# Kernel optimization log

Measured on AMD Instinct MI355X. Metric: run time of the kernel, lower is better.

Reference implementation:

```python
import jax, jax.numpy as jnp
import numpy as np

D = 1024
H = 16
HD = D // H
EPS = 1e-5


def layer_norm(x, g, b):
    mu = jnp.mean(x, axis=-1, keepdims=True)
    var = jnp.var(x, axis=-1, keepdims=True)
    return (x - mu) * jax.lax.rsqrt(var + EPS) * g + b


def setup_inputs() -> dict:
    key = jax.random.key(0)
    ks = jax.random.split(key, 16)
    s = 0.02
    return {
        "x": jax.random.normal(ks[0], (2, 2048, D), jnp.float32),
        "ln1_g": jnp.ones((D,), jnp.float32),
        "ln1_b": jnp.zeros((D,), jnp.float32),
        "Wq": jax.random.normal(ks[1], (D, D), jnp.float32) * s,
        "bq": jnp.zeros((D,), jnp.float32),
        "Wk": jax.random.normal(ks[2], (D, D), jnp.float32) * s,
        "bk": jnp.zeros((D,), jnp.float32),
        "Wv": jax.random.normal(ks[3], (D, D), jnp.float32) * s,
        "bv": jnp.zeros((D,), jnp.float32),
        "Wo": jax.random.normal(ks[4], (D, D), jnp.float32) * s,
        "bo": jnp.zeros((D,), jnp.float32),
        "ln2_g": jnp.ones((D,), jnp.float32),
        "ln2_b": jnp.zeros((D,), jnp.float32),
        "W1": jax.random.normal(ks[5], (D, 4 * D), jnp.float32) * s,
        "b1": jnp.zeros((4 * D,), jnp.float32),
        "W2": jax.random.normal(ks[6], (4 * D, D), jnp.float32) * s,
        "b2": jnp.zeros((D,), jnp.float32),
    }


def reference(x, ln1_g, ln1_b, Wq, bq, Wk, bk, Wv, bv, Wo, bo, ln2_g, ln2_b, W1, b1, W2, b2):
    B, T, _ = x.shape
    # --- attention sub-block (pre-LN) ---
    h = layer_norm(x, ln1_g, ln1_b)
    q = (h @ Wq + bq).reshape(B, T, H, HD).transpose(0, 2, 1, 3)  # [B,H,T,hd]
    k = (h @ Wk + bk).reshape(B, T, H, HD).transpose(0, 2, 1, 3)
    v = (h @ Wv + bv).reshape(B, T, H, HD).transpose(0, 2, 1, 3)
    scores = jnp.einsum("bhqd,bhkd->bhqk", q, k)  # full O(T^2) scores as in source
    causal = jnp.tril(jnp.ones((T, T), bool))
    scores = jnp.where(causal, scores, -jnp.inf)
    w = jax.nn.softmax(scores / np.sqrt(HD), axis=-1)
    ctx = jnp.einsum("bhqk,bhkd->bhqd", w, v)
    ctx = ctx.transpose(0, 2, 1, 3).reshape(B, T, D)
    x = x + (ctx @ Wo + bo)
    # --- MLP sub-block (pre-LN) ---
    h = layer_norm(x, ln2_g, ln2_b)
    h = jax.nn.gelu(h @ W1 + b1, approximate=False)
    x = x + (h @ W2 + b2)
    return x
```

## Files before the change

kernel.cpp:

```cpp
#include <hip/hip_runtime.h>
#include <math.h>


typedef _Float16 half8 __attribute__((ext_vector_type(8)));
typedef _Float16 half4v __attribute__((ext_vector_type(4)));
typedef float floatx4 __attribute__((ext_vector_type(4)));

#define DMODEL 1024
#define SEQT   2048
#define NTOK   4096
#define NHEAD  16
#define HDIM   64

__device__ __forceinline__ void llds16(const _Float16* g, _Float16* l) {
  __builtin_amdgcn_global_load_lds(
      (const __attribute__((address_space(1))) void*)g,
      (__attribute__((address_space(3))) void*)l, 16, 0, 0);
}

__global__ __launch_bounds__(256) void wtrans_kernel(
    const float* __restrict__ Wq, const float* __restrict__ Wk,
    const float* __restrict__ Wv, const float* __restrict__ Wo,
    const float* __restrict__ W1, const float* __restrict__ W2,
    _Float16* __restrict__ wt_base) {
  __shared__ float tilebuf[32][33];
  int id = blockIdx.x;
  const float* src; _Float16* dst; int K, N, t;
  if (id < 4096) {
    int s = id >> 10;
    src = (s == 0) ? Wq : (s == 1) ? Wk : (s == 2) ? Wv : Wo;
    dst = wt_base + (size_t)s * (1024 * 1024);
    K = 1024; N = 1024; t = id & 1023;
  } else if (id < 8192) {
    src = W1; dst = wt_base + (size_t)4 * 1024 * 1024; K = 1024; N = 4096; t = id - 4096;
  } else {
    src = W2; dst = wt_base + (size_t)8 * 1024 * 1024; K = 4096; N = 1024; t = id - 8192;
  }
  int tilesN = N >> 5;
  int tk = t / tilesN, tn = t % tilesN;
  int c = threadIdx.x & 31, r0 = threadIdx.x >> 5;
#pragma unroll
  for (int i = 0; i < 4; ++i) {
    int r = r0 + i * 8;
    tilebuf[r][c] = src[(size_t)(tk * 32 + r) * N + tn * 32 + c];
  }
  __syncthreads();
#pragma unroll
  for (int i = 0; i < 4; ++i) {
    int r = r0 + i * 8;
    dst[(size_t)(tn * 32 + r) * K + tk * 32 + c] = (_Float16)tilebuf[c][r];
  }
}

__global__ __launch_bounds__(256) void ln_kernel(
    const float* __restrict__ x, const float* __restrict__ g,
    const float* __restrict__ b, _Float16* __restrict__ out) {
  int row = blockIdx.x;
  int t = threadIdx.x;
  const float4 xv = ((const float4*)(x + (size_t)row * DMODEL))[t];
  float s = xv.x + xv.y + xv.z + xv.w;
  float s2 = xv.x * xv.x + xv.y * xv.y + xv.z * xv.z + xv.w * xv.w;
#pragma unroll
  for (int off = 32; off; off >>= 1) {
    s += __shfl_down(s, off);
    s2 += __shfl_down(s2, off);
  }
  __shared__ float red[8];
  int wid = t >> 6;
  if ((t & 63) == 0) { red[wid] = s; red[wid + 4] = s2; }
  __syncthreads();
  s = red[0] + red[1] + red[2] + red[3];
  s2 = red[4] + red[5] + red[6] + red[7];
  float mu = s * (1.0f / DMODEL);
  float var = s2 * (1.0f / DMODEL) - mu * mu;
  float rstd = rsqrtf(var + 1e-5f);
  const float4 gv = ((const float4*)g)[t];
  const float4 bv = ((const float4*)b)[t];
  half4v o;
  o[0] = (_Float16)((xv.x - mu) * rstd * gv.x + bv.x);
  o[1] = (_Float16)((xv.y - mu) * rstd * gv.y + bv.y);
  o[2] = (_Float16)((xv.z - mu) * rstd * gv.z + bv.z);
  o[3] = (_Float16)((xv.w - mu) * rstd * gv.w + bv.w);
  *(half4v*)(out + (size_t)row * DMODEL + t * 4) = o;
}

template <int MODE>
__global__ __launch_bounds__(256) void gemm_kernel(
    const _Float16* __restrict__ A, const _Float16* __restrict__ Bt0, int K,
    const float* __restrict__ bias0, const float* __restrict__ bias1,
    const float* __restrict__ bias2, const float* __restrict__ res,
    float* __restrict__ outf, _Float16* __restrict__ outh) {
  constexpr int NT = (MODE == 1) ? 64 : 128;
  constexpr int MI = (NT == 128) ? 4 : 2;
  constexpr int BCH = NT / 64;
  __shared__ __align__(16) _Float16 As[2][128 * 32];
  __shared__ __align__(16) _Float16 Bs[2][NT * 32];
  const int tid = threadIdx.x;
  const int m0 = blockIdx.x * 128;
  const _Float16* Bt;
  const float* bias;
  _Float16* outh_sel = outh;
  int n0, sel = 0;
  if (MODE == 0) {
    sel = blockIdx.y >> 3;
    n0 = (blockIdx.y & 7) * 128;
    Bt = Bt0 + (size_t)sel * (1024 * 1024);
    bias = (sel == 0) ? bias0 : (sel == 1) ? bias1 : bias2;
    outh_sel = outh + (size_t)sel * ((size_t)NTOK * DMODEL);
  } else {
    n0 = blockIdx.y * NT;
    Bt = Bt0;
    bias = bias0;
  }
  const int w = tid >> 6, lane = tid & 63;
  const int l15 = lane & 15, q8 = lane >> 4;
  const int wrow = (NT == 128) ? (w >> 1) * 64 : w * 32;
  const int wcol = (NT == 128) ? (w & 1) * 64 : 0;
  const int csw = (q8 ^ ((l15 >> 1) & 3)) * 8;

  const _Float16* gA[2]; int ldsA[2];
  const _Float16* gB[BCH]; int ldsB[BCH];
#pragma unroll
  for (int i = 0; i < 2; ++i) {
    int c0 = i * 256 + w * 64;
    int idx = c0 + lane;
    int m = idx >> 2;
    int kq = ((idx & 3) ^ ((m >> 1) & 3)) * 8;
    gA[i] = A + (size_t)(m0 + m) * K + kq;
    ldsA[i] = c0 * 8;
  }
#pragma unroll
  for (int i = 0; i < BCH; ++i) {
    int c0 = i * 256 + w * 64;
    int idx = c0 + lane;
    int m = idx >> 2;
    int kq = ((idx & 3) ^ ((m >> 1) & 3)) * 8;
    gB[i] = Bt + (size_t)(n0 + m) * K + kq;
    ldsB[i] = c0 * 8;
  }

  auto stage = [&](int buf) {
#pragma unroll
    for (int i = 0; i < 2; ++i) {
      llds16(gA[i], &As[buf][ldsA[i]]);
      gA[i] += 32;
    }
#pragma unroll
    for (int i = 0; i < BCH; ++i) {
      llds16(gB[i], &Bs[buf][ldsB[i]]);
      gB[i] += 32;
    }
  };

  floatx4 acc[MI][4];
#pragma unroll
  for (int i = 0; i < MI; ++i)
#pragma unroll
    for (int j = 0; j < 4; ++j) acc[i][j] = (floatx4){0.f, 0.f, 0.f, 0.f};

  const int nk = K >> 5;
  stage(0);
  __syncthreads();
  for (int t = 0; t < nk; ++t) {
    const int buf = t & 1;
    if (t + 1 < nk) stage(buf ^ 1);
    half8 af[MI], bf[4];
#pragma unroll
    for (int i = 0; i < MI; ++i)
      af[i] = *(const half8*)&As[buf][(wrow + i * 16 + l15) * 32 + csw];
#pragma unroll
    for (int j = 0; j < 4; ++j)
      bf[j] = *(const half8*)&Bs[buf][(wcol + j * 16 + l15) * 32 + csw];
#pragma unroll
    for (int i = 0; i < MI; ++i)
#pragma unroll
      for (int j = 0; j < 4; ++j)
        acc[i][j] = __builtin_amdgcn_mfma_f32_16x16x32_f16(af[i], bf[j], acc[i][j], 0, 0, 0);
    __syncthreads();
  }

#pragma unroll
  for (int i = 0; i < MI; ++i) {
    int rowb = m0 + wrow + i * 16 + q8 * 4;
#pragma unroll
    for (int j = 0; j < 4; ++j) {
      int col = n0 + wcol + j * 16 + l15;
      float bval = bias[col];
#pragma unroll
      for (int r = 0; r < 4; ++r) {
        int row = rowb + r;
        float v = acc[i][j][r] + bval;
        if (MODE == 0) {
          int bb = row >> 11, tt = row & 2047;
          int hh = col >> 6, hd = col & 63;
          if (sel == 2)
            outh_sel[((size_t)(bb * NHEAD + hh) * HDIM + hd) * SEQT + tt] = (_Float16)v;
          else
            outh_sel[((size_t)(bb * NHEAD + hh) * SEQT + tt) * HDIM + hd] = (_Float16)v;
        } else if (MODE == 1) {
          v += res[(size_t)row * 1024 + col];
          outf[(size_t)row * 1024 + col] = v;
        } else {
          float z = 1.5957691216f * v * (1.0f + 0.044715f * v * v);
          float gl = v / (1.0f + __expf(-z));
          outh[(size_t)row * 4096 + col] = (_Float16)gl;
        }
      }
    }
  }
}

__global__ __launch_bounds__(256) void attn_kernel(
    const _Float16* __restrict__ q, const _Float16* __restrict__ k,
    const _Float16* __restrict__ vt, _Float16* __restrict__ ctx) {
  __shared__ __align__(16) _Float16 Ks[2][64 * 64];
  __shared__ __align__(16) _Float16 Vs[2][64 * 64];
  __shared__ __align__(16) _Float16 Ps[64 * 72];
  __shared__ float Lpart[4][64];
  const int tid = threadIdx.x;
  const int w = tid >> 6, lane = tid & 63;
  const int l15 = lane & 15, q8 = lane >> 4;
  const int bh = blockIdx.y;
  const int pr = blockIdx.x;
  const size_t base = (size_t)bh * SEQT * HDIM;

  const _Float16* gk0[2]; const _Float16* gv0[2]; int ldsc[2];
#pragma unroll
  for (int i = 0; i < 2; ++i) {
    int c = i * 256 + w * 64 + lane;
    int r = c >> 3, gc = ((c & 7) ^ (r & 7)) * 8;
    gk0[i] = k + base + (size_t)r * HDIM + gc;
    gv0[i] = vt + base + (size_t)r * SEQT + gc;
    ldsc[i] = c * 8;
  }
  auto stage = [&](int kt, int buf) {
#pragma unroll
    for (int i = 0; i < 2; ++i) {
      llds16(gk0[i] + (size_t)kt * (64 * HDIM), &Ks[buf][ldsc[i]]);
      llds16(gv0[i] + kt * 64, &Vs[buf][ldsc[i]]);
    }
  };

  const int rswA = (l15 & 7);
  const int cs0 = (q8 ^ rswA) * 8;
  const int cs1 = ((4 + q8) ^ rswA) * 8;

  int s = 0;
  stage(0, 0);
  __syncthreads();
  for (int ph = 0; ph < 2; ++ph) {
    const int qtile = ph ? 31 - pr : pr;
    const int ntile = qtile + 1;
    half8 bq[4][2];
#pragma unroll
    for (int nt = 0; nt < 4; ++nt) {
      const half8* qp = (const half8*)(q + base + (size_t)(qtile * 64 + nt * 16 + l15) * HDIM);
      bq[nt][0] = qp[q8];
      bq[nt][1] = qp[4 + q8];
    }
    floatx4 acc[4];
#pragma unroll
    for (int j = 0; j < 4; ++j) acc[j] = (floatx4){0.f, 0.f, 0.f, 0.f};
    float lsum[4] = {0.f, 0.f, 0.f, 0.f};

    for (int jt = 0; jt < ntile; ++jt, ++s) {
      const int buf = s & 1;
      if (s + 1 < 33) {
        int sn = s + 1;
        int nkt = (sn <= pr) ? sn : sn - (pr + 1);
        stage(nkt, buf ^ 1);
      }
      half8 ak0 = *(const half8*)&Ks[buf][(w * 16 + l15) * 64 + cs0];
      half8 ak1 = *(const half8*)&Ks[buf][(w * 16 + l15) * 64 + cs1];
      floatx4 sv[4];
#pragma unroll
      for (int nt = 0; nt < 4; ++nt) {
        sv[nt] = __builtin_amdgcn_mfma_f32_16x16x32_f16(ak0, bq[nt][0],
                                                        (floatx4){0.f, 0.f, 0.f, 0.f}, 0, 0, 0);
        sv[nt] = __builtin_amdgcn_mfma_f32_16x16x32_f16(ak1, bq[nt][1], sv[nt], 0, 0, 0);
      }
      const bool diag = (jt == ntile - 1);
#pragma unroll
      for (int nt = 0; nt < 4; ++nt) {
        half4v phv;
#pragma unroll
        for (int r = 0; r < 4; ++r) {
          float p = __expf(sv[nt][r] * 0.125f);
          if (diag) {
            p = (w * 16 + q8 * 4 + r <= nt * 16 + l15) ? p : 0.f;
          }
          lsum[nt] += p;
          phv[r] = (_Float16)p;
        }
        *(half4v*)&Ps[(nt * 16 + l15) * 72 + w * 16 + q8 * 4] = phv;
      }
      __syncthreads();
      half8 ap0 = *(const half8*)&Ps[(w * 16 + l15) * 72 + q8 * 8];
      half8 ap1 = *(const half8*)&Ps[(w * 16 + l15) * 72 + 32 + q8 * 8];
#pragma unroll
      for (int ntd = 0; ntd < 4; ++ntd) {
        half8 bv0 = *(const half8*)&Vs[buf][(ntd * 16 + l15) * 64 + cs0];
        half8 bv1 = *(const half8*)&Vs[buf][(ntd * 16 + l15) * 64 + cs1];
        acc[ntd] = __builtin_amdgcn_mfma_f32_16x16x32_f16(ap0, bv0, acc[ntd], 0, 0, 0);
        acc[ntd] = __builtin_amdgcn_mfma_f32_16x16x32_f16(ap1, bv1, acc[ntd], 0, 0, 0);
      }
      __syncthreads();
    }

#pragma unroll
    for (int nt = 0; nt < 4; ++nt) {
      lsum[nt] += __shfl_xor(lsum[nt], 16);
      lsum[nt] += __shfl_xor(lsum[nt], 32);
      if (q8 == 0) Lpart[w][nt * 16 + l15] = lsum[nt];
    }
    __syncthreads();
    const int b = bh >> 4, h = bh & 15;
#pragma unroll
    for (int r = 0; r < 4; ++r) {
      int qr = w * 16 + q8 * 4 + r;
      float inv = 1.0f / (Lpart[0][qr] + Lpart[1][qr] + Lpart[2][qr] + Lpart[3][qr]);
      int tg = qtile * 64 + qr;
      _Float16* op = ctx + ((size_t)(b * SEQT + tg)) * DMODEL + h * HDIM;
#pragma unroll
      for (int ntd = 0; ntd < 4; ++ntd)
        op[ntd * 16 + l15] = (_Float16)(acc[ntd][r] * inv);
    }
  }
}

extern "C" void kernel_launch(void* const* d_in, const int* in_sizes, int n_in,
                              void* d_out, int out_size, void* d_ws, size_t ws_size,
                              hipStream_t stream) {
  (void)in_sizes; (void)n_in; (void)out_size; (void)ws_size;
  const float* x    = (const float*)d_in[0];
  const float* ln1g = (const float*)d_in[1];
  const float* ln1b = (const float*)d_in[2];
  const float* Wq   = (const float*)d_in[3];
  const float* bq   = (const float*)d_in[4];
  const float* Wk   = (const float*)d_in[5];
  const float* bk   = (const float*)d_in[6];
  const float* Wv   = (const float*)d_in[7];
  const float* bv   = (const float*)d_in[8];
  const float* Wo   = (const float*)d_in[9];
  const float* bo   = (const float*)d_in[10];
  const float* ln2g = (const float*)d_in[11];
  const float* ln2b = (const float*)d_in[12];
  const float* W1   = (const float*)d_in[13];
  const float* b1   = (const float*)d_in[14];
  const float* W2   = (const float*)d_in[15];
  const float* b2   = (const float*)d_in[16];
  float* out = (float*)d_out;

  char* ws = (char*)d_ws;
  _Float16* wt    = (_Float16*)(ws);
  _Float16* h16   = (_Float16*)(ws + ((size_t)24 << 20));
  _Float16* qkv   = (_Float16*)(ws + ((size_t)32 << 20));
  _Float16* ctx16 = (_Float16*)(ws + ((size_t)24 << 20));
  float*    x1    = (float*)   (ws + ((size_t)32 << 20));
  _Float16* h2    = (_Float16*)(ws + ((size_t)48 << 20));
  _Float16* mid   = (_Float16*)(ws + ((size_t)56 << 20));

  const size_t QKV1 = (size_t)NTOK * DMODEL;

  wtrans_kernel<<<12288, 256, 0, stream>>>(Wq, Wk, Wv, Wo, W1, W2, wt);
  ln_kernel<<<NTOK, 256, 0, stream>>>(x, ln1g, ln1b, h16);
  gemm_kernel<0><<<dim3(32, 24), 256, 0, stream>>>(
      h16, wt, 1024, bq, bk, bv, nullptr, nullptr, qkv);
  attn_kernel<<<dim3(16, 32), 256, 0, stream>>>(
      qkv, qkv + QKV1, qkv + 2 * QKV1, ctx16);
  gemm_kernel<1><<<dim3(32, 16), 256, 0, stream>>>(
      ctx16, wt + (size_t)3 * 1024 * 1024, 1024, bo, nullptr, nullptr, x, x1, nullptr);
  ln_kernel<<<NTOK, 256, 0, stream>>>(x1, ln2g, ln2b, h2);
  gemm_kernel<2><<<dim3(32, 32), 256, 0, stream>>>(
      h2, wt + (size_t)4 * 1024 * 1024, 1024, b1, nullptr, nullptr, nullptr, nullptr, mid);
  gemm_kernel<1><<<dim3(32, 16), 256, 0, stream>>>(
      mid, wt + (size_t)8 * 1024 * 1024, 4096, b2, nullptr, nullptr, x1, out, nullptr);
}
```

Baseline: 355.4 us.

## Use 4-deep LDS pipeline with single barrier for MODE 1 GEMM

For the MODE 1 GEMM (NT=64), the LDS staging grows from double to quadruple buffering with a prefetch distance of two. Explicit vmcnt waits plus one s_barrier per iteration replace the trailing __syncthreads, letting global-to-LDS loads overlap more compute. In the attention kernel, a __syncthreads is replaced by an lgkmcnt wait and a raw barrier, which leaves outstanding global loads unwaited. This costs more LDS per block and depends on the hand-counted vmcnt values matching the number of loads each stage issues.

```diff
diff --git a/kernel.cpp b/kernel.cpp
--- a/kernel.cpp
+++ b/kernel.cpp
@@ -93,8 +93,9 @@
   constexpr int NT = (MODE == 1) ? 64 : 128;
   constexpr int MI = (NT == 128) ? 4 : 2;
   constexpr int BCH = NT / 64;
-  __shared__ __align__(16) _Float16 As[2][128 * 32];
-  __shared__ __align__(16) _Float16 Bs[2][NT * 32];
+  constexpr int NBUF = (MODE == 1) ? 4 : 2;
+  __shared__ __align__(16) _Float16 As[NBUF][128 * 32];
+  __shared__ __align__(16) _Float16 Bs[NBUF][NT * 32];
   const int tid = threadIdx.x;
   const int m0 = blockIdx.x * 128;
   const _Float16* Bt;
@@ -159,24 +160,55 @@
     for (int j = 0; j < 4; ++j) acc[i][j] = (floatx4){0.f, 0.f, 0.f, 0.f};
 
   const int nk = K >> 5;
-  stage(0);
-  __syncthreads();
-  for (int t = 0; t < nk; ++t) {
-    const int buf = t & 1;
-    if (t + 1 < nk) stage(buf ^ 1);
-    half8 af[MI], bf[4];
-#pragma unroll
-    for (int i = 0; i < MI; ++i)
-      af[i] = *(const half8*)&As[buf][(wrow + i * 16 + l15) * 32 + csw];
-#pragma unroll
-    for (int j = 0; j < 4; ++j)
-      bf[j] = *(const half8*)&Bs[buf][(wcol + j * 16 + l15) * 32 + csw];
-#pragma unroll
-    for (int i = 0; i < MI; ++i)
+  if constexpr (MODE == 1) {
+    stage(0);
+    stage(1);
+    for (int t = 0; t < nk; ++t) {
+      const int buf = t & 3;
+      if (t + 2 < nk) {
+        stage((t + 2) & 3);
+        asm volatile("s_waitcnt vmcnt(6)" ::: "memory");
+      } else if (t + 1 < nk) {
+        asm volatile("s_waitcnt vmcnt(3)" ::: "memory");
+      } else {
+        asm volatile("s_waitcnt vmcnt(0)" ::: "memory");
+      }
+      __builtin_amdgcn_s_barrier();
+      asm volatile("" ::: "memory");
+      half8 af[MI], bf[4];
+#pragma unroll
+      for (int i = 0; i < MI; ++i)
+        af[i] = *(const half8*)&As[buf][(wrow + i * 16 + l15) * 32 + csw];
 #pragma unroll
       for (int j = 0; j < 4; ++j)
-        acc[i][j] = __builtin_amdgcn_mfma_f32_16x16x32_f16(af[i], bf[j], acc[i][j], 0, 0, 0);
+        bf[j] = *(const half8*)&Bs[buf][(wcol + j * 16 + l15) * 32 + csw];
+#pragma unroll
+      for (int i = 0; i < MI; ++i)
+#pragma unroll
+        for (int j = 0; j < 4; ++j)
+          acc[i][j] = __builtin_amdgcn_mfma_f32_16x16x32_f16(af[i], bf[j], acc[i][j], 0, 0, 0);
+      asm volatile("" ::: "memory");
+    }
+  } else {
+    stage(0);
     __syncthreads();
+    for (int t = 0; t < nk; ++t) {
+      const int buf = t & 1;
+      if (t + 1 < nk) stage(buf ^ 1);
+      half8 af[MI], bf[4];
+#pragma unroll
+      for (int i = 0; i < MI; ++i)
+        af[i] = *(const half8*)&As[buf][(wrow + i * 16 + l15) * 32 + csw];
+#pragma unroll
+      for (int j = 0; j < 4; ++j)
+        bf[j] = *(const half8*)&Bs[buf][(wcol + j * 16 + l15) * 32 + csw];
+#pragma unroll
+      for (int i = 0; i < MI; ++i)
+#pragma unroll
+        for (int j = 0; j < 4; ++j)
+          acc[i][j] = __builtin_amdgcn_mfma_f32_16x16x32_f16(af[i], bf[j], acc[i][j], 0, 0, 0);
+      __syncthreads();
+    }
   }
 
 #pragma unroll
@@ -294,7 +326,9 @@
         }
         *(half4v*)&Ps[(nt * 16 + l15) * 72 + w * 16 + q8 * 4] = phv;
       }
-      __syncthreads();
+      asm volatile("s_waitcnt lgkmcnt(0)" ::: "memory");
+      __builtin_amdgcn_s_barrier();
+      asm volatile("" ::: "memory");
       half8 ap0 = *(const half8*)&Ps[(w * 16 + l15) * 72 + q8 * 8];
       half8 ap1 = *(const half8*)&Ps[(w * 16 + l15) * 72 + 32 + q8 * 8];
 #pragma unroll
```

After: 354.2 us. About the same (-0.3%).

## Add 256x256-tile pipelined GEMM for MLP with split-K down-projection

Applied to the files above, without the earlier changes.

Adds a new 512-thread GEMM kernel with 256x256 tiles, K-step 64, XOR-swizzled LDS staged by direct global-to-LDS loads, and phased MFMA quadrants under barriers and s_setprio. It replaces both MLP GEMMs. The W2 GEMM is split four ways along K, with three partial sums stored in fp16 and added by a new reduction kernel. The attention kernel's post-P-store __syncthreads is swapped for an explicit lgkmcnt wait plus s_barrier. The aim is more data reuse per tile and better MFMA/load overlap, at the cost of an extra launch, extra partial-sum traffic and fp16 rounding of the partials.

```diff
diff --git a/kernel.cpp b/kernel.cpp
--- a/kernel.cpp
+++ b/kernel.cpp
@@ -82,6 +82,184 @@
   o[2] = (_Float16)((xv.z - mu) * rstd * gv.z + bv.z);
   o[3] = (_Float16)((xv.w - mu) * rstd * gv.w + bv.w);
   *(half4v*)(out + (size_t)row * DMODEL + t * 4) = o;
+}
+
+template <int OUTMODE>
+__global__ __launch_bounds__(512, 2) void gemm256_kernel(
+    const _Float16* __restrict__ A, const _Float16* __restrict__ Bt, int K,
+    const float* __restrict__ bias, const float* __restrict__ res,
+    float* __restrict__ outf, _Float16* __restrict__ outh,
+    _Float16* __restrict__ p1, _Float16* __restrict__ p2,
+    _Float16* __restrict__ p3) {
+  __shared__ __align__(16) _Float16 As[2][256 * 64];
+  __shared__ __align__(16) _Float16 Bs[2][256 * 64];
+  const int tid = threadIdx.x;
+  const int w = tid >> 6, lane = tid & 63;
+  const int l15 = lane & 15, q8 = lane >> 4;
+  const int wr = w >> 2, wc = w & 3;
+  const int m0 = blockIdx.x * 256;
+  const int n0 = blockIdx.y * 256;
+  int Keff = K, koff = 0;
+  if (OUTMODE == 1) { Keff = K >> 2; koff = blockIdx.z * Keff; }
+  const int nk = Keff >> 6;
+
+  auto stage_half = [&](int kt, int buf, int h) {
+#pragma unroll
+    for (int o = 0; o < 2; ++o) {
+      int cl = o * 512 + tid;
+      int rr = cl >> 3;
+      int m = h * 128 + rr;
+      int sc = (cl & 7) ^ (m & 7);
+      llds16(A + (size_t)(m0 + m) * K + koff + kt * 64 + sc * 8,
+             &As[buf][h * 8192 + cl * 8]);
+    }
+#pragma unroll
+    for (int o = 0; o < 2; ++o) {
+      int cl = o * 512 + tid;
+      int rr = cl >> 3;
+      int m = h * 128 + rr;
+      int sc = (cl & 7) ^ (m & 7);
+      llds16(Bt + (size_t)(n0 + m) * K + koff + kt * 64 + sc * 8,
+             &Bs[buf][h * 8192 + cl * 8]);
+    }
+  };
+
+  floatx4 acc[8][4];
+#pragma unroll
+  for (int i = 0; i < 8; ++i)
+#pragma unroll
+    for (int j = 0; j < 4; ++j) acc[i][j] = (floatx4){0.f, 0.f, 0.f, 0.f};
+
+  half8 a[4][2], b[2][2];
+
+#define DSA(BUF, R2)                                                         \
+  {                                                                          \
+    _Pragma("unroll") for (int i = 0; i < 4; ++i) {                          \
+      int rA = wr * 128 + (R2)*64 + i * 16 + l15;                            \
+      _Pragma("unroll") for (int kh = 0; kh < 2; ++kh) {                     \
+        int slot = (kh * 4 + q8) ^ (rA & 7);                                 \
+        a[i][kh] = *(const half8*)&As[BUF][rA * 64 + slot * 8];              \
+      }                                                                      \
+    }                                                                        \
+  }
+#define DSB(BUF, C2)                                                         \
+  {                                                                          \
+    _Pragma("unroll") for (int j = 0; j < 2; ++j) {                          \
+      int rB = wc * 64 + (C2)*32 + j * 16 + l15;                             \
+      _Pragma("unroll") for (int kh = 0; kh < 2; ++kh) {                     \
+        int slot = (kh * 4 + q8) ^ (rB & 7);                                 \
+        b[j][kh] = *(const half8*)&Bs[BUF][rB * 64 + slot * 8];              \
+      }                                                                      \
+    }                                                                        \
+  }
+#define MFMAQ(R2, C2)                                                        \
+  {                                                                          \
+    _Pragma("unroll") for (int i = 0; i < 4; ++i)                            \
+        _Pragma("unroll") for (int j = 0; j < 2; ++j)                        \
+            _Pragma("unroll") for (int kh = 0; kh < 2; ++kh)                 \
+                acc[(R2)*4 + i][(C2)*2 + j] =                                \
+        __builtin_amdgcn_mfma_f32_16x16x32_f16(a[i][kh], b[j][kh],           \
+                                               acc[(R2)*4 + i][(C2)*2 + j], \
+                                               0, 0, 0);                     \
+  }
+#define PH_SYNC()                                           \
+  __builtin_amdgcn_s_barrier();                             \
+  asm volatile("s_waitcnt lgkmcnt(0)" ::: "memory");        \
+  __builtin_amdgcn_sched_barrier(0);                        \
+  __builtin_amdgcn_s_setprio(1);
+#define PH_END()                                            \
+  __builtin_amdgcn_s_setprio(0);                            \
+  __builtin_amdgcn_s_barrier();
+
+  stage_half(0, 0, 0);
+  stage_half(0, 0, 1);
+  if (nk > 1) {
+    stage_half(1, 1, 0);
+    asm volatile("s_waitcnt vmcnt(4)" ::: "memory");
+  } else {
+    asm volatile("s_waitcnt vmcnt(0)" ::: "memory");
+  }
+  __builtin_amdgcn_s_barrier();
+
+  for (int kt = 0; kt < nk; ++kt) {
+    const int buf = kt & 1;
+    DSA(buf, 0);
+    DSB(buf, 0);
+    if (kt + 1 < nk) stage_half(kt + 1, buf ^ 1, 1);
+    PH_SYNC();
+    MFMAQ(0, 0);
+    PH_END();
+    DSB(buf, 1);
+    PH_SYNC();
+    MFMAQ(0, 1);
+    PH_END();
+    DSA(buf, 1);
+    DSB(buf, 0);
+    PH_SYNC();
+    MFMAQ(1, 0);
+    PH_END();
+    DSB(buf, 1);
+    PH_SYNC();
+    MFMAQ(1, 1);
+    __builtin_amdgcn_s_setprio(0);
+    __builtin_amdgcn_s_barrier();
+    if (kt + 2 < nk) stage_half(kt + 2, buf, 0);
+    if (kt + 1 < nk) {
+      asm volatile("s_waitcnt vmcnt(4)" ::: "memory");
+    } else {
+      asm volatile("s_waitcnt vmcnt(0)" ::: "memory");
+    }
+    __builtin_amdgcn_s_barrier();
+  }
+#undef DSA
+#undef DSB
+#undef MFMAQ
+#undef PH_SYNC
+#undef PH_END
+
+#pragma unroll
+  for (int fi = 0; fi < 8; ++fi) {
+    int rowb = m0 + wr * 128 + fi * 16 + q8 * 4;
+#pragma unroll
+    for (int fj = 0; fj < 4; ++fj) {
+      int col = n0 + wc * 64 + fj * 16 + l15;
+      float bval = bias[col];
+#pragma unroll
+      for (int r = 0; r < 4; ++r) {
+        int row = rowb + r;
+        float v = acc[fi][fj][r];
+        if (OUTMODE == 0) {
+          v += bval;
+          float z = 1.5957691216f * v * (1.0f + 0.044715f * v * v);
+          float gl = v / (1.0f + __expf(-z));
+          outh[(size_t)row * 4096 + col] = (_Float16)gl;
+        } else {
+          if (blockIdx.z == 0) {
+            v += bval + res[(size_t)row * 1024 + col];
+            outf[(size_t)row * 1024 + col] = v;
+          } else {
+            _Float16* pp = (blockIdx.z == 1) ? p1 : (blockIdx.z == 2) ? p2 : p3;
+            pp[(size_t)row * 1024 + col] = (_Float16)v;
+          }
+        }
+      }
+    }
+  }
+}
+
+__global__ __launch_bounds__(256) void redux_kernel(
+    float* __restrict__ out, const _Float16* __restrict__ p1,
+    const _Float16* __restrict__ p2, const _Float16* __restrict__ p3) {
+  size_t i = ((size_t)blockIdx.x * 256 + threadIdx.x) * 4;
+  float4 o = *(float4*)(out + i);
+  half4v a = *(const half4v*)(p1 + i);
+  half4v b = *(const half4v*)(p2 + i);
+  half4v c = *(const half4v*)(p3 + i);
+  o.x += (float)a[0] + (float)b[0] + (float)c[0];
+  o.y += (float)a[1] + (float)b[1] + (float)c[1];
+  o.z += (float)a[2] + (float)b[2] + (float)c[2];
+  o.w += (float)a[3] + (float)b[3] + (float)c[3];
+  *(float4*)(out + i) = o;
 }
 
 template <int MODE>
@@ -197,13 +375,9 @@
             outh_sel[((size_t)(bb * NHEAD + hh) * HDIM + hd) * SEQT + tt] = (_Float16)v;
           else
             outh_sel[((size_t)(bb * NHEAD + hh) * SEQT + tt) * HDIM + hd] = (_Float16)v;
-        } else if (MODE == 1) {
+        } else {
           v += res[(size_t)row * 1024 + col];
           outf[(size_t)row * 1024 + col] = v;
-        } else {
-          float z = 1.5957691216f * v * (1.0f + 0.044715f * v * v);
-          float gl = v / (1.0f + __expf(-z));
-          outh[(size_t)row * 4096 + col] = (_Float16)gl;
         }
       }
     }
@@ -294,7 +468,9 @@
         }
         *(half4v*)&Ps[(nt * 16 + l15) * 72 + w * 16 + q8 * 4] = phv;
       }
-      __syncthreads();
+      asm volatile("s_waitcnt lgkmcnt(0)" ::: "memory");
+      __builtin_amdgcn_s_barrier();
+      asm volatile("" ::: "memory");
       half8 ap0 = *(const half8*)&Ps[(w * 16 + l15) * 72 + q8 * 8];
       half8 ap1 = *(const half8*)&Ps[(w * 16 + l15) * 72 + 32 + q8 * 8];
 #pragma unroll
@@ -359,6 +535,9 @@
   float*    x1    = (float*)   (ws + ((size_t)32 << 20));
   _Float16* h2    = (_Float16*)(ws + ((size_t)48 << 20));
   _Float16* mid   = (_Float16*)(ws + ((size_t)56 << 20));
+  _Float16* part1 = (_Float16*)(ws + ((size_t)8 << 20));
+  _Float16* part2 = (_Float16*)(ws + ((size_t)24 << 20));
+  _Float16* part3 = (_Float16*)(ws + ((size_t)48 << 20));
 
   const size_t QKV1 = (size_t)NTOK * DMODEL;
 
@@ -371,8 +550,11 @@
   gemm_kernel<1><<<dim3(32, 16), 256, 0, stream>>>(
       ctx16, wt + (size_t)3 * 1024 * 1024, 1024, bo, nullptr, nullptr, x, x1, nullptr);
   ln_kernel<<<NTOK, 256, 0, stream>>>(x1, ln2g, ln2b, h2);
-  gemm_kernel<2><<<dim3(32, 32), 256, 0, stream>>>(
-      h2, wt + (size_t)4 * 1024 * 1024, 1024, b1, nullptr, nullptr, nullptr, nullptr, mid);
-  gemm_kernel<1><<<dim3(32, 16), 256, 0, stream>>>(
-      mid, wt + (size_t)8 * 1024 * 1024, 4096, b2, nullptr, nullptr, x1, out, nullptr);
-}
+  gemm256_kernel<0><<<dim3(16, 16), 512, 0, stream>>>(
+      h2, wt + (size_t)4 * 1024 * 1024, 1024, b1, nullptr, nullptr, mid,
+      nullptr, nullptr, nullptr);
+  gemm256_kernel<1><<<dim3(16, 4, 4), 512, 0, stream>>>(
+      mid, wt + (size_t)8 * 1024 * 1024, 4096, b2, x1, out, nullptr,
+      part1, part2, part3);
+  redux_kernel<<<4096, 256, 0, stream>>>(out, part1, part2, part3);
+}
```

Result: slower. 374.1 us (+5.2%).
